# Kernel tuning notes

Measured on AMD Instinct MI355X. Metric: run time of the kernel, lower is better.

The kernel has to match this reference:

```python
import jax, jax.numpy as jnp
import numpy as np

BN_EPS = 1e-5


def _bn(h, gamma, beta):
    # torch BatchNorm1d training-mode forward: biased batch variance
    mu = h.mean(axis=0)
    var = h.var(axis=0)
    return (h - mu) * jax.lax.rsqrt(var + BN_EPS) * gamma + beta


def setup_inputs() -> dict:
    N, E, H = 100000, 1600000, 128
    HID = 2 * H  # get_torch_mlp hidden_channels = 2*out_channels = 256
    key = jax.random.key(0)
    ks = jax.random.split(key, 8)
    s_lin = 1.0 / np.sqrt(H)
    s_mlp = 1.0 / np.sqrt(2 * H)
    return {
        "x": jax.random.normal(ks[0], (N, H), dtype=jnp.float32),
        "edge_index": jax.random.randint(ks[1], (2, E), 0, N, dtype=jnp.int64),
        "lin_w": jax.random.normal(ks[2], (2 * H, H), dtype=jnp.float32) * s_lin,
        "lin_b": jnp.zeros((2 * H,), dtype=jnp.float32),
        "eps": jnp.zeros((), dtype=jnp.float32),
        "w1": jax.random.normal(ks[3], (HID, 2 * H), dtype=jnp.float32) * s_mlp,
        "g1": jnp.ones((HID,), dtype=jnp.float32),
        "b1": jnp.zeros((HID,), dtype=jnp.float32),
        "w2": jax.random.normal(ks[4], (HID, HID), dtype=jnp.float32) * (1.0 / np.sqrt(HID)),
        "g2": jnp.ones((HID,), dtype=jnp.float32),
        "b2": jnp.zeros((HID,), dtype=jnp.float32),
        "w3": jax.random.normal(ks[5], (H, HID), dtype=jnp.float32) * (1.0 / np.sqrt(HID)),
        "b3": jnp.zeros((H,), dtype=jnp.float32),
    }


def reference(x, edge_index, lin_w, lin_b, eps, w1, g1, b1, w2, g2, b2, w3, b3):
    N = x.shape[0]
    dst, src = edge_index[0], edge_index[1]
    # transfer1(atoms, G): irregular gather of neighbor rows + scatter-add,
    # duplicated across the two order-1 linmap channel blocks -> [N, 2H]
    agg = jax.ops.segment_sum(x[src], dst, num_segments=N)
    x_transfer = jnp.concatenate([agg, agg], axis=-1)
    # linmaps1 on singleton domains: [broadcast(sum)=x, id=x] -> [N, 2H]
    x_linmaps = jnp.concatenate([x, x], axis=-1)
    x_lin = x @ lin_w.T + lin_b
    h = x_lin + (1.0 + eps) * x_linmaps + x_transfer  # stack([...]).sum(0)
    # MLP: Linear(no bias) -> BN -> ReLU -> Linear(no bias) -> BN -> ReLU -> Linear(bias)
    h = jax.nn.relu(_bn(h @ w1.T, g1, b1))
    h = jax.nn.relu(_bn(h @ w2.T, g2, b2))
    h = h @ w3.T + b3
    return h  # rows of the output ptensors1 (same atoms)
```

## Files before the change

### kernel.cpp

```cpp
#include <hip/hip_runtime.h>
#include <cstdint>
#include <cstddef>

typedef __bf16 bf16_t;
typedef __bf16 bf16x8 __attribute__((ext_vector_type(8)));
typedef float f32x4 __attribute__((ext_vector_type(4)));

#define GLOBAL_AS __attribute__((address_space(1)))
#define LDS_AS    __attribute__((address_space(3)))

__device__ __forceinline__ void glds16(const void* g, void* l) {
    __builtin_amdgcn_global_load_lds((const GLOBAL_AS void*)g, (LDS_AS void*)l, 16, 0, 0);
}

__global__ void conv_k(const float* __restrict__ in, bf16_t* __restrict__ out, int n8) {
    int id = blockIdx.x * 256 + threadIdx.x;
    if (id >= n8) return;
    const float4* p = (const float4*)in;
    float4 a = p[2 * id], b = p[2 * id + 1];
    bf16x8 o;
    o[0] = (bf16_t)a.x; o[1] = (bf16_t)a.y; o[2] = (bf16_t)a.z; o[3] = (bf16_t)a.w;
    o[4] = (bf16_t)b.x; o[5] = (bf16_t)b.y; o[6] = (bf16_t)b.z; o[7] = (bf16_t)b.w;
    *(bf16x8*)(out + (size_t)id * 8) = o;
}

__global__ void conv_x_k(const float* __restrict__ in, bf16_t* __restrict__ ha, int n8) {
    int id = blockIdx.x * 256 + threadIdx.x;
    if (id >= n8) return;
    const float4* p = (const float4*)in;
    float4 a = p[2 * id], b = p[2 * id + 1];
    bf16x8 o;
    o[0] = (bf16_t)a.x; o[1] = (bf16_t)a.y; o[2] = (bf16_t)a.z; o[3] = (bf16_t)a.w;
    o[4] = (bf16_t)b.x; o[5] = (bf16_t)b.y; o[6] = (bf16_t)b.z; o[7] = (bf16_t)b.w;
    int row = id >> 4, ch = id & 15;
    *(bf16x8*)(ha + (size_t)row * 256 + ch * 8) = o;
}

__global__ void wcomb_k(const float* __restrict__ w1, const float* __restrict__ lin_w,
                        const float* __restrict__ lin_b, const float* __restrict__ eps_p,
                        bf16_t* __restrict__ wc, float* __restrict__ bcomb) {
    __shared__ float red[256];
    int c = blockIdx.x, t = threadIdx.x;
    const float* w1row = w1 + c * 256;
    float onepe = 1.f + *eps_p;
    float v;
    if (t < 128) {
        float acc = 0.f;
        for (int j = 0; j < 256; j++) acc += w1row[j] * lin_w[j * 128 + t];
        v = acc + onepe * (w1row[t] + w1row[t + 128]);
    } else {
        int m = t - 128;
        v = w1row[m] + w1row[t];
    }
    wc[c * 256 + t] = (bf16_t)v;
    red[t] = w1row[t] * lin_b[t];
    __syncthreads();
    for (int off = 128; off > 0; off >>= 1) {
        if (t < off) red[t] += red[t + off];
        __syncthreads();
    }
    if (t == 0) bcomb[c] = red[0];
}

__global__ void detect_k(const int* __restrict__ ei, int* __restrict__ flag) {
    int v = ei[2 * threadIdx.x + 1];
    if (v != 0) atomicOr(flag, 1);
}

#define CHUNK 8192

__global__ __launch_bounds__(256) void bhist_k(const void* __restrict__ ei, const int* __restrict__ flag,
                                               int E, int* __restrict__ bcnt) {
    __shared__ int cnt[1024];
    int t = threadIdx.x;
    for (int b = t; b < 1024; b += 256) cnt[b] = 0;
    __syncthreads();
    int base = blockIdx.x * CHUNK;
    int i32 = *flag;
#pragma unroll 4
    for (int i = 0; i < CHUNK / 256; i++) {
        int e = base + t + 256 * i;
        if (e < E) {
            int dst = i32 ? ((const int*)ei)[e] : (int)((const long long*)ei)[e];
            atomicAdd(&cnt[dst >> 7], 1);
        }
    }
    __syncthreads();
    for (int b = t; b < 1024; b += 256)
        if (cnt[b]) atomicAdd(&bcnt[b], cnt[b]);
}

__global__ __launch_bounds__(1024) void bscan_k(const int* __restrict__ bcnt, int* __restrict__ boffs,
                                                int* __restrict__ gcur, int* __restrict__ offs,
                                                int NBK, int N, int E) {
    __shared__ int lds[1024];
    int t = threadIdx.x;
    int v = (t < NBK) ? bcnt[t] : 0;
    lds[t] = v;
    __syncthreads();
    for (int off = 1; off < 1024; off <<= 1) {
        int add = (t >= off) ? lds[t - off] : 0;
        __syncthreads();
        lds[t] += add;
        __syncthreads();
    }
    if (t < NBK) {
        int excl = lds[t] - v;
        boffs[t] = excl;
        gcur[t] = excl;
    }
    if (t == 0) { boffs[NBK] = E; offs[N] = E; }
}

__global__ __launch_bounds__(256) void binfill_k(const void* __restrict__ ei, const int* __restrict__ flag,
                                                 int E, int NBK, int* __restrict__ gcur,
                                                 unsigned* __restrict__ pairs) {
    __shared__ int cnt[1024];
    __shared__ int pref[1024];
    __shared__ int cur[1024];
    __shared__ int gbase[1024];
    __shared__ int red[256];
    __shared__ unsigned slot[CHUNK];
    __shared__ unsigned short sbk[CHUNK];
    int t = threadIdx.x;
    int base = blockIdx.x * CHUNK;
    int chunk_n = E - base; if (chunk_n > CHUNK) chunk_n = CHUNK;
    int i32 = *flag;
    for (int b = t; b < 1024; b += 256) cnt[b] = 0;
    __syncthreads();
#pragma unroll 4
    for (int i = 0; i < CHUNK / 256; i++) {
        int e = base + t + 256 * i;
        if (e < E) {
            int dst = i32 ? ((const int*)ei)[e] : (int)((const long long*)ei)[e];
            atomicAdd(&cnt[dst >> 7], 1);
        }
    }
    __syncthreads();
    int t4 = t * 4;
    int c0 = cnt[t4], c1 = cnt[t4 + 1], c2 = cnt[t4 + 2], c3 = cnt[t4 + 3];
    int s = c0 + c1 + c2 + c3;
    red[t] = s;
    __syncthreads();
    for (int off = 1; off < 256; off <<= 1) {
        int add = (t >= off) ? red[t - off] : 0;
        __syncthreads();
        red[t] += add;
        __syncthreads();
    }
    int run = red[t] - s;
    pref[t4] = run; cur[t4] = run; run += c0;
    pref[t4 + 1] = run; cur[t4 + 1] = run; run += c1;
    pref[t4 + 2] = run; cur[t4 + 2] = run; run += c2;
    pref[t4 + 3] = run; cur[t4 + 3] = run;
    __syncthreads();
#pragma unroll 4
    for (int i = 0; i < CHUNK / 256; i++) {
        int e = base + t + 256 * i;
        if (e < E) {
            int dst, src;
            if (i32) { dst = ((const int*)ei)[e]; src = ((const int*)ei)[E + e]; }
            else     { dst = (int)((const long long*)ei)[e]; src = (int)((const long long*)ei)[E + e]; }
            int b = dst >> 7;
            int p = atomicAdd(&cur[b], 1);
            slot[p] = ((unsigned)(dst & 127) << 20) | (unsigned)src;
            sbk[p] = (unsigned short)b;
        }
    }
    __syncthreads();
    for (int b = t; b < 1024; b += 256) {
        int c = (b + 1 < 1024) ? (pref[b + 1] - pref[b]) : (chunk_n - pref[b]);
        if (b < NBK && c > 0) gbase[b] = atomicAdd(&gcur[b], c);
    }
    __syncthreads();
    for (int i = t; i < chunk_n; i += 256) {
        int bk = sbk[i];
        pairs[gbase[bk] + (i - pref[bk])] = slot[i];
    }
}

__global__ __launch_bounds__(256) void bsort2_k(const unsigned* __restrict__ pairs,
                                                const int* __restrict__ boffs,
                                                int* __restrict__ offs,
                                                int* __restrict__ csr, int N) {
    __shared__ int cnt[128], pref[128], cur[128];
    int t = threadIdx.x;
    int b = blockIdx.x;
    int s = boffs[b], e = boffs[b + 1];
    if (t < 128) cnt[t] = 0;
    __syncthreads();
    for (int i = s + t; i < e; i += 256)
        atomicAdd(&cnt[pairs[i] >> 20], 1);
    __syncthreads();
    if (t < 128) pref[t] = cnt[t];
    __syncthreads();
    for (int off = 1; off < 128; off <<= 1) {
        int v = 0;
        if (t < 128 && t >= off) v = pref[t - off];
        __syncthreads();
        if (t < 128) pref[t] += v;
        __syncthreads();
    }
    if (t < 128) {
        int ex = pref[t] - cnt[t];
        cur[t] = ex;
        int node = b * 128 + t;
        if (node < N) offs[node] = s + ex;
    }
    __syncthreads();
    for (int i = s + t; i < e; i += 256) {
        unsigned u = pairs[i];
        int dl = (int)(u >> 20);
        int p = atomicAdd(&cur[dl], 1);
        csr[s + p] = (int)(u & 0xFFFFFu);
    }
}

__global__ __launch_bounds__(256) void gather_k(bf16_t* __restrict__ ha, const int* __restrict__ offs,
                                                const int* __restrict__ csr, int N) {
    int w = (blockIdx.x * 256 + threadIdx.x) >> 6;
    if (w >= N) return;
    int lane = threadIdx.x & 63;
    int g = lane >> 4, l15 = lane & 15;
    int s = offs[w], e = offs[w + 1];
    float acc[8] = {0.f, 0.f, 0.f, 0.f, 0.f, 0.f, 0.f, 0.f};
    float acc2[8] = {0.f, 0.f, 0.f, 0.f, 0.f, 0.f, 0.f, 0.f};
    int i = s + g;
    bool h0 = i < e, h1 = i + 4 < e;
    int p0 = h0 ? csr[i] : 0;
    int p1 = h1 ? csr[i + 4] : 0;
    while (h1) {
        int ni = i + 8;
        bool nh0 = ni < e, nh1 = ni + 4 < e;
        int np0 = nh0 ? csr[ni] : 0;
        int np1 = nh1 ? csr[ni + 4] : 0;
        bf16x8 v0 = *(const bf16x8*)(ha + (size_t)p0 * 256 + l15 * 8);
        bf16x8 v1 = *(const bf16x8*)(ha + (size_t)p1 * 256 + l15 * 8);
#pragma unroll
        for (int j = 0; j < 8; j++) { acc[j] += (float)v0[j]; acc2[j] += (float)v1[j]; }
        i = ni; p0 = np0; p1 = np1; h0 = nh0; h1 = nh1;
    }
    if (h0) {
        bf16x8 v0 = *(const bf16x8*)(ha + (size_t)p0 * 256 + l15 * 8);
#pragma unroll
        for (int j = 0; j < 8; j++) acc[j] += (float)v0[j];
    }
#pragma unroll
    for (int j = 0; j < 8; j++) {
        acc[j] += acc2[j];
        acc[j] += __shfl_xor(acc[j], 16);
        acc[j] += __shfl_xor(acc[j], 32);
    }
    if (g == 0) {
        bf16x8 o;
#pragma unroll
        for (int j = 0; j < 8; j++) o[j] = (bf16_t)acc[j];
        *(bf16x8*)(ha + (size_t)w * 256 + 128 + l15 * 8) = o;
    }
}

template<int NHALF, bool BNIN, bool STATS, bool FINAL, bool BIAS>
__global__ __launch_bounds__(512, 1) void gemm_w(
    const bf16_t* __restrict__ A, const bf16_t* __restrict__ W,
    const float2* __restrict__ scsh2,
    float* __restrict__ sums, float* __restrict__ sqs,
    const float* __restrict__ bias,
    bf16_t* __restrict__ Obf, float* __restrict__ Of, int N, int ntiles, int tstride)
{
    constexpr int NCOLTOT = NHALF * 128;
    __shared__ __align__(16) char smemW[65536];
    __shared__ __align__(16) char smemA[2][32768];

    const int tid = threadIdx.x;
    const int lane = tid & 63, wid = tid >> 6;
    const int l15 = lane & 15, l4 = lane >> 4;
    const int rowg = wid & 1, colg = wid >> 1;
    const int colh = (NHALF == 2) ? (int)(blockIdx.x >> 7) : 0;
    const int rb   = (NHALF == 2) ? (int)(blockIdx.x & 127) : (int)blockIdx.x;

#pragma unroll
    for (int it = 0; it < 8; it++) {
        int d = (it * 512 + tid) * 16;
        int col = d >> 9, koff = d & 511;
        int ksw = koff ^ ((col & 7) << 4);
        glds16((const char*)W + (size_t)(colh * 128 + col) * 512 + ksw, smemW + d);
    }

    auto stageA = [&](int buf, int t) {
        size_t rowbase = (size_t)t * 64;
#pragma unroll
        for (int it = 0; it < 4; it++) {
            int d = (it * 512 + tid) * 16;
            int row = d >> 9, koff = d & 511;
            int ksw = koff ^ ((row & 7) << 4);
            glds16((const char*)A + (rowbase + row) * 512 + ksw, smemA[buf] + d);
        }
    };

    float2 sslr[32];
    if constexpr (BNIN) {
#pragma unroll
        for (int it = 0; it < 4; it++) {
            int d = (it * 512 + tid) * 16;
            int row = d >> 9;
            int k0 = ((d & 511) ^ ((row & 7) << 4)) >> 1;
#pragma unroll
            for (int i = 0; i < 8; i++) sslr[it * 8 + i] = scsh2[k0 + i];
        }
    }

    auto transformA = [&](int buf) {
#pragma unroll
        for (int it = 0; it < 4; it++) {
            int d = (it * 512 + tid) * 16;
            bf16x8 v = *(const bf16x8*)(smemA[buf] + d);
            bf16x8 o;
#pragma unroll
            for (int i = 0; i < 8; i++) {
                float2 ss = sslr[it * 8 + i];
                o[i] = (bf16_t)fmaxf((float)v[i] * ss.x + ss.y, 0.f);
            }
            *(bf16x8*)(smemA[buf] + d) = o;
        }
    };

    float bbv[2];
    if constexpr (BIAS || FINAL) {
#pragma unroll
        for (int cf = 0; cf < 2; cf++)
            bbv[cf] = bias[colh * 128 + colg * 32 + cf * 16 + l15];
    }
    float sA[2], qA[2];
    if constexpr (STATS) { sA[0] = sA[1] = qA[0] = qA[1] = 0.f; }

    auto compute = [&](int buf, f32x4 (&acc)[2][2]) {
#pragma unroll
        for (int i = 0; i < 2; i++) { acc[i][0] = f32x4{0.f,0.f,0.f,0.f}; acc[i][1] = f32x4{0.f,0.f,0.f,0.f}; }
#pragma unroll
        for (int c = 0; c < 8; c++) {
            const int koff = c * 64 + l4 * 16;
            bf16x8 a[2];
#pragma unroll
            for (int fr = 0; fr < 2; fr++) {
                int row = rowg * 32 + fr * 16 + l15;
                a[fr] = *(const bf16x8*)(smemA[buf] + row * 512 + (koff ^ ((row & 7) << 4)));
            }
#pragma unroll
            for (int cf = 0; cf < 2; cf++) {
                int col = colg * 32 + cf * 16 + l15;
                const bf16x8 b = *(const bf16x8*)(smemW + col * 512 + (koff ^ ((col & 7) << 4)));
                acc[0][cf] = __builtin_amdgcn_mfma_f32_16x16x32_bf16(a[0], b, acc[0][cf], 0, 0, 0);
                acc[1][cf] = __builtin_amdgcn_mfma_f32_16x16x32_bf16(a[1], b, acc[1][cf], 0, 0, 0);
            }
        }
    };

    auto epilogue = [&](int t, f32x4 (&acc)[2][2]) {
        const int rows0 = t * 64 + rowg * 32;
#pragma unroll
        for (int fr = 0; fr < 2; fr++) {
            int rb0 = rows0 + fr * 16 + l4 * 4;
#pragma unroll
            for (int cf = 0; cf < 2; cf++) {
                int colw = colh * 128 + colg * 32 + cf * 16 + l15;
                f32x4 av = acc[fr][cf];
#pragma unroll
                for (int i = 0; i < 4; i++) {
                    int r = rb0 + i;
                    if constexpr (FINAL) {
                        if (r < N) Of[(size_t)r * NCOLTOT + colw] = av[i] + bbv[cf];
                    } else {
                        float v = av[i];
                        if constexpr (BIAS) v += bbv[cf];
                        bf16_t hv = (bf16_t)v;
                        if (r < N) Obf[(size_t)r * 256 + colw] = hv;
                        if constexpr (STATS) {
                            float vv = (r < N) ? (float)hv : 0.f;
                            sA[cf] += vv; qA[cf] += vv * vv;
                        }
                    }
                }
            }
        }
    };

    f32x4 accP[2][2], accQ[2][2];
    int t = rb, buf = 0;
    if (t < ntiles) stageA(0, t);
    __syncthreads();
    if constexpr (BNIN) {
        if (t < ntiles) transformA(0);
        __syncthreads();
    }

    int tprev = -1;
    bool ping = true;
    while (t < ntiles) {
        int tn = t + tstride;
        if (tn < ntiles) stageA(buf ^ 1, tn);
        if (tprev >= 0) {
            if (ping) epilogue(tprev, accQ); else epilogue(tprev, accP);
        }
        if (ping) compute(buf, accP); else compute(buf, accQ);
        __syncthreads();
        if constexpr (BNIN) {
            if (tn < ntiles) transformA(buf ^ 1);
            __syncthreads();
        }
        tprev = t; t = tn; buf ^= 1; ping = !ping;
    }
    if (tprev >= 0) {
        if (ping) epilogue(tprev, accQ); else epilogue(tprev, accP);
    }

    if constexpr (STATS) {
#pragma unroll
        for (int cf = 0; cf < 2; cf++) {
            float s = sA[cf], q = qA[cf];
            s += __shfl_xor(s, 16); s += __shfl_xor(s, 32);
            q += __shfl_xor(q, 16); q += __shfl_xor(q, 32);
            if (lane < 16) {
                int colw = colh * 128 + colg * 32 + cf * 16 + l15;
                atomicAdd(&sums[colw], s);
                atomicAdd(&sqs[colw], q);
            }
        }
    }
}

__global__ void finalize_k(const float* __restrict__ sum, const float* __restrict__ sq,
                           const float* __restrict__ g, const float* __restrict__ b,
                           float2* __restrict__ scsh2, float invN) {
    int t = threadIdx.x;
    float mean = sum[t] * invN;
    float var = sq[t] * invN - mean * mean;
    float s = g[t] * rsqrtf(var + 1e-5f);
    scsh2[t] = make_float2(s, b[t] - mean * s);
}

extern "C" void kernel_launch(void* const* d_in, const int* in_sizes, int n_in,
                              void* d_out, int out_size, void* d_ws, size_t ws_size,
                              hipStream_t stream)
{
    const int N = in_sizes[0] / 128;
    const int E = in_sizes[1] / 2;
    const float* x     = (const float*)d_in[0];
    const void*  ei    = d_in[1];
    const float* lin_w = (const float*)d_in[2];
    const float* lin_b = (const float*)d_in[3];
    const float* eps   = (const float*)d_in[4];
    const float* w1    = (const float*)d_in[5];
    const float* g1    = (const float*)d_in[6];
    const float* b1    = (const float*)d_in[7];
    const float* w2    = (const float*)d_in[8];
    const float* g2    = (const float*)d_in[9];
    const float* b2    = (const float*)d_in[10];
    const float* w3    = (const float*)d_in[11];
    const float* b3    = (const float*)d_in[12];
    float* out = (float*)d_out;

    char* ws = (char*)d_ws;
    size_t o = 0;
    auto alloc = [&](size_t bytes) -> char* {
        char* p = ws + o;
        o = (o + bytes + 255) & ~(size_t)255;
        return p;
    };
    bf16_t*   ha    = (bf16_t*)alloc((size_t)N * 256 * 2);
    bf16_t*   hb    = (bf16_t*)alloc((size_t)N * 256 * 2);
    bf16_t*   wcb   = (bf16_t*)alloc((size_t)256 * 256 * 2);
    bf16_t*   w2b   = (bf16_t*)alloc((size_t)256 * 256 * 2);
    bf16_t*   w3b   = (bf16_t*)alloc((size_t)128 * 256 * 2);
    float*    bcomb = (float*)alloc(256 * 4);
    float*    stats = (float*)alloc(4 * 256 * 4);
    float2*   scsh1 = (float2*)alloc(256 * 8);
    float2*   scsh2 = (float2*)alloc(256 * 8);
    int*      bcnt  = (int*)alloc(1024 * 4);
    int*      boffs = (int*)alloc(1025 * 4);
    int*      gcur  = (int*)alloc(1024 * 4);
    int*      offs  = (int*)alloc((size_t)(N + 1) * 4);
    unsigned* pairs = (unsigned*)alloc((size_t)E * 4);
    int*      csr   = (int*)alloc((size_t)E * 4);
    int*      flag  = (int*)alloc(4);

    const int NBK = (N + 127) >> 7;

    hipMemsetAsync(bcnt, 0, 1024 * 4, stream);
    hipMemsetAsync(stats, 0, 4 * 256 * 4, stream);
    hipMemsetAsync(flag, 0, 4, stream);

    int nx8 = N * 16;
    conv_x_k<<<(nx8 + 255) / 256, 256, 0, stream>>>(x, ha, nx8);
    wcomb_k<<<256, 256, 0, stream>>>(w1, lin_w, lin_b, eps, wcb, bcomb);
    conv_k<<<32, 256, 0, stream>>>(w2, w2b, 8192);
    conv_k<<<16, 256, 0, stream>>>(w3, w3b, 4096);

    const int nch = (E + CHUNK - 1) / CHUNK;
    detect_k<<<1, 256, 0, stream>>>((const int*)ei, flag);
    bhist_k<<<nch, 256, 0, stream>>>(ei, flag, E, bcnt);
    bscan_k<<<1, 1024, 0, stream>>>(bcnt, boffs, gcur, offs, NBK, N, E);
    binfill_k<<<nch, 256, 0, stream>>>(ei, flag, E, NBK, gcur, pairs);
    bsort2_k<<<NBK, 256, 0, stream>>>(pairs, boffs, offs, csr, N);
    gather_k<<<(N + 3) / 4, 256, 0, stream>>>(ha, offs, csr, N);

    const int nt64 = (N + 63) / 64;
    gemm_w<2, false, true, false, true><<<256, 512, 0, stream>>>(
        ha, wcb, nullptr, stats + 0, stats + 256, bcomb, hb, nullptr, N, nt64, 128);
    finalize_k<<<1, 256, 0, stream>>>(stats + 0, stats + 256, g1, b1, scsh1, 1.f / (float)N);
    gemm_w<2, true, true, false, false><<<256, 512, 0, stream>>>(
        hb, w2b, scsh1, stats + 512, stats + 768, nullptr, ha, nullptr, N, nt64, 128);
    finalize_k<<<1, 256, 0, stream>>>(stats + 512, stats + 768, g2, b2, scsh2, 1.f / (float)N);
    gemm_w<1, true, false, true, true><<<256, 512, 0, stream>>>(
        ha, w3b, scsh2, nullptr, nullptr, b3, nullptr, out, N, nt64, 256);
}
```

Before: 250.8 us.

## Split GEMM columns into 64-wide quarters, single-buffer A, raise occupancy

```diff
diff --git a/kernel.cpp b/kernel.cpp
--- a/kernel.cpp
+++ b/kernel.cpp
@@ -259,41 +259,41 @@
     }
 }
 
-template<int NHALF, bool BNIN, bool STATS, bool FINAL, bool BIAS>
-__global__ __launch_bounds__(512, 1) void gemm_w(
+template<int NCOLTOT, bool BNIN, bool STATS, bool FINAL, bool BIAS>
+__global__ __launch_bounds__(512, 4) void gemm_q(
     const bf16_t* __restrict__ A, const bf16_t* __restrict__ W,
     const float2* __restrict__ scsh2,
     float* __restrict__ sums, float* __restrict__ sqs,
     const float* __restrict__ bias,
-    bf16_t* __restrict__ Obf, float* __restrict__ Of, int N, int ntiles, int tstride)
+    bf16_t* __restrict__ Obf, float* __restrict__ Of, int N, int ntiles, int shift)
 {
-    constexpr int NCOLTOT = NHALF * 128;
-    __shared__ __align__(16) char smemW[65536];
-    __shared__ __align__(16) char smemA[2][32768];
+    __shared__ __align__(16) char smemW[32768];
+    __shared__ __align__(16) char smemA[32768];
 
     const int tid = threadIdx.x;
     const int lane = tid & 63, wid = tid >> 6;
     const int l15 = lane & 15, l4 = lane >> 4;
     const int rowg = wid & 1, colg = wid >> 1;
-    const int colh = (NHALF == 2) ? (int)(blockIdx.x >> 7) : 0;
-    const int rb   = (NHALF == 2) ? (int)(blockIdx.x & 127) : (int)blockIdx.x;
-
-#pragma unroll
-    for (int it = 0; it < 8; it++) {
+    const int tstride = 1 << shift;
+    const int colq = (int)blockIdx.x >> shift;
+    const int rb = (int)blockIdx.x & (tstride - 1);
+
+#pragma unroll
+    for (int it = 0; it < 4; it++) {
         int d = (it * 512 + tid) * 16;
         int col = d >> 9, koff = d & 511;
         int ksw = koff ^ ((col & 7) << 4);
-        glds16((const char*)W + (size_t)(colh * 128 + col) * 512 + ksw, smemW + d);
-    }
-
-    auto stageA = [&](int buf, int t) {
+        glds16((const char*)W + (size_t)(colq * 64 + col) * 512 + ksw, smemW + d);
+    }
+
+    auto stageA = [&](int t) {
         size_t rowbase = (size_t)t * 64;
 #pragma unroll
         for (int it = 0; it < 4; it++) {
             int d = (it * 512 + tid) * 16;
             int row = d >> 9, koff = d & 511;
             int ksw = koff ^ ((row & 7) << 4);
-            glds16((const char*)A + (rowbase + row) * 512 + ksw, smemA[buf] + d);
+            glds16((const char*)A + (rowbase + row) * 512 + ksw, smemA + d);
         }
     };
 
@@ -309,121 +309,102 @@
         }
     }
 
-    auto transformA = [&](int buf) {
+    auto transformA = [&]() {
 #pragma unroll
         for (int it = 0; it < 4; it++) {
             int d = (it * 512 + tid) * 16;
-            bf16x8 v = *(const bf16x8*)(smemA[buf] + d);
+            bf16x8 v = *(const bf16x8*)(smemA + d);
             bf16x8 o;
 #pragma unroll
             for (int i = 0; i < 8; i++) {
                 float2 ss = sslr[it * 8 + i];
                 o[i] = (bf16_t)fmaxf((float)v[i] * ss.x + ss.y, 0.f);
             }
-            *(bf16x8*)(smemA[buf] + d) = o;
+            *(bf16x8*)(smemA + d) = o;
         }
     };
 
-    float bbv[2];
-    if constexpr (BIAS || FINAL) {
-#pragma unroll
-        for (int cf = 0; cf < 2; cf++)
-            bbv[cf] = bias[colh * 128 + colg * 32 + cf * 16 + l15];
-    }
-    float sA[2], qA[2];
-    if constexpr (STATS) { sA[0] = sA[1] = qA[0] = qA[1] = 0.f; }
-
-    auto compute = [&](int buf, f32x4 (&acc)[2][2]) {
-#pragma unroll
-        for (int i = 0; i < 2; i++) { acc[i][0] = f32x4{0.f,0.f,0.f,0.f}; acc[i][1] = f32x4{0.f,0.f,0.f,0.f}; }
+    const int colw = colq * 64 + colg * 16 + l15;
+    float bbv = 0.f;
+    if constexpr (BIAS || FINAL) bbv = bias[colw];
+    float sA = 0.f, qA = 0.f;
+
+    f32x4 acc[2];
+
+    auto compute = [&]() {
+        acc[0] = f32x4{0.f, 0.f, 0.f, 0.f};
+        acc[1] = f32x4{0.f, 0.f, 0.f, 0.f};
+        const int col = colg * 16 + l15;
+        const int wsw = (col & 7) << 4;
 #pragma unroll
         for (int c = 0; c < 8; c++) {
             const int koff = c * 64 + l4 * 16;
-            bf16x8 a[2];
-#pragma unroll
-            for (int fr = 0; fr < 2; fr++) {
-                int row = rowg * 32 + fr * 16 + l15;
-                a[fr] = *(const bf16x8*)(smemA[buf] + row * 512 + (koff ^ ((row & 7) << 4)));
+            bf16x8 a0, a1;
+            {
+                int row = rowg * 32 + l15;
+                a0 = *(const bf16x8*)(smemA + row * 512 + (koff ^ ((row & 7) << 4)));
+                row += 16;
+                a1 = *(const bf16x8*)(smemA + row * 512 + (koff ^ ((row & 7) << 4)));
             }
-#pragma unroll
-            for (int cf = 0; cf < 2; cf++) {
-                int col = colg * 32 + cf * 16 + l15;
-                const bf16x8 b = *(const bf16x8*)(smemW + col * 512 + (koff ^ ((col & 7) << 4)));
-                acc[0][cf] = __builtin_amdgcn_mfma_f32_16x16x32_bf16(a[0], b, acc[0][cf], 0, 0, 0);
-                acc[1][cf] = __builtin_amdgcn_mfma_f32_16x16x32_bf16(a[1], b, acc[1][cf], 0, 0, 0);
-            }
+            const bf16x8 b = *(const bf16x8*)(smemW + col * 512 + (koff ^ wsw));
+            acc[0] = __builtin_amdgcn_mfma_f32_16x16x32_bf16(a0, b, acc[0], 0, 0, 0);
+            acc[1] = __builtin_amdgcn_mfma_f32_16x16x32_bf16(a1, b, acc[1], 0, 0, 0);
         }
     };
 
-    auto epilogue = [&](int t, f32x4 (&acc)[2][2]) {
+    auto epilogue = [&](int t) {
         const int rows0 = t * 64 + rowg * 32;
 #pragma unroll
         for (int fr = 0; fr < 2; fr++) {
             int rb0 = rows0 + fr * 16 + l4 * 4;
-#pragma unroll
-            for (int cf = 0; cf < 2; cf++) {
-                int colw = colh * 128 + colg * 32 + cf * 16 + l15;
-                f32x4 av = acc[fr][cf];
-#pragma unroll
-                for (int i = 0; i < 4; i++) {
-                    int r = rb0 + i;
-                    if constexpr (FINAL) {
-                        if (r < N) Of[(size_t)r * NCOLTOT + colw] = av[i] + bbv[cf];
-                    } else {
-                        float v = av[i];
-                        if constexpr (BIAS) v += bbv[cf];
-                        bf16_t hv = (bf16_t)v;
-                        if (r < N) Obf[(size_t)r * 256 + colw] = hv;
-                        if constexpr (STATS) {
-                            float vv = (r < N) ? (float)hv : 0.f;
-                            sA[cf] += vv; qA[cf] += vv * vv;
-                        }
+            f32x4 av = acc[fr];
+#pragma unroll
+            for (int i = 0; i < 4; i++) {
+                int r = rb0 + i;
+                if constexpr (FINAL) {
+                    if (r < N) Of[(size_t)r * NCOLTOT + colw] = av[i] + bbv;
+                } else {
+                    float v = av[i];
+                    if constexpr (BIAS) v += bbv;
+                    bf16_t hv = (bf16_t)v;
+                    if (r < N) Obf[(size_t)r * 256 + colw] = hv;
+                    if constexpr (STATS) {
+                        float vv = (r < N) ? (float)hv : 0.f;
+                        sA += vv; qA += vv * vv;
                     }
                 }
             }
         }
     };
 
-    f32x4 accP[2][2], accQ[2][2];
-    int t = rb, buf = 0;
-    if (t < ntiles) stageA(0, t);
+    int t = rb;
+    if (t < ntiles) stageA(t);
     __syncthreads();
     if constexpr (BNIN) {
-        if (t < ntiles) transformA(0);
-        __syncthreads();
-    }
-
-    int tprev = -1;
-    bool ping = true;
+        if (t < ntiles) transformA();
+        __syncthreads();
+    }
+
     while (t < ntiles) {
+        compute();
+        __syncthreads();
         int tn = t + tstride;
-        if (tn < ntiles) stageA(buf ^ 1, tn);
-        if (tprev >= 0) {
-            if (ping) epilogue(tprev, accQ); else epilogue(tprev, accP);
-        }
-        if (ping) compute(buf, accP); else compute(buf, accQ);
+        if (tn < ntiles) stageA(tn);
+        epilogue(t);
         __syncthreads();
         if constexpr (BNIN) {
-            if (tn < ntiles) transformA(buf ^ 1);
+            if (tn < ntiles) transformA();
             __syncthreads();
         }
-        tprev = t; t = tn; buf ^= 1; ping = !ping;
-    }
-    if (tprev >= 0) {
-        if (ping) epilogue(tprev, accQ); else epilogue(tprev, accP);
+        t = tn;
     }
 
     if constexpr (STATS) {
-#pragma unroll
-        for (int cf = 0; cf < 2; cf++) {
-            float s = sA[cf], q = qA[cf];
-            s += __shfl_xor(s, 16); s += __shfl_xor(s, 32);
-            q += __shfl_xor(q, 16); q += __shfl_xor(q, 32);
-            if (lane < 16) {
-                int colw = colh * 128 + colg * 32 + cf * 16 + l15;
-                atomicAdd(&sums[colw], s);
-                atomicAdd(&sqs[colw], q);
-            }
+        sA += __shfl_xor(sA, 16); sA += __shfl_xor(sA, 32);
+        qA += __shfl_xor(qA, 16); qA += __shfl_xor(qA, 32);
+        if (lane < 16) {
+            atomicAdd(&sums[colw], sA);
+            atomicAdd(&sqs[colw], qA);
         }
     }
 }
@@ -504,12 +485,12 @@
     gather_k<<<(N + 3) / 4, 256, 0, stream>>>(ha, offs, csr, N);
 
     const int nt64 = (N + 63) / 64;
-    gemm_w<2, false, true, false, true><<<256, 512, 0, stream>>>(
-        ha, wcb, nullptr, stats + 0, stats + 256, bcomb, hb, nullptr, N, nt64, 128);
+    gemm_q<256, false, true, false, true><<<512, 512, 0, stream>>>(
+        ha, wcb, nullptr, stats + 0, stats + 256, bcomb, hb, nullptr, N, nt64, 7);
     finalize_k<<<1, 256, 0, stream>>>(stats + 0, stats + 256, g1, b1, scsh1, 1.f / (float)N);
-    gemm_w<2, true, true, false, false><<<256, 512, 0, stream>>>(
-        hb, w2b, scsh1, stats + 512, stats + 768, nullptr, ha, nullptr, N, nt64, 128);
+    gemm_q<256, true, true, false, false><<<512, 512, 0, stream>>>(
+        hb, w2b, scsh1, stats + 512, stats + 768, nullptr, ha, nullptr, N, nt64, 7);
     finalize_k<<<1, 256, 0, stream>>>(stats + 512, stats + 768, g2, b2, scsh2, 1.f / (float)N);
-    gemm_w<1, true, false, true, true><<<256, 512, 0, stream>>>(
-        ha, w3b, scsh2, nullptr, nullptr, b3, nullptr, out, N, nt64, 256);
-}
+    gemm_q<128, true, false, true, true><<<512, 512, 0, stream>>>(
+        ha, w3b, scsh2, nullptr, nullptr, b3, nullptr, out, N, nt64, 8);
+}
```

Measured after the change: 242.5 us. -3.3%, faster.
